# Kernel tuning notes

Measured on AMD Instinct MI355X. Metric: run time of the kernel, lower is better.

The kernel has to match this reference:

```python
import jax, jax.numpy as jnp
import numpy as np

DIM = 1024
HEADS = 16
HEAD_DIM = DIM // HEADS
RPE_K = 16
B, T = 4, 1024


def setup_inputs() -> dict:
    key = jax.random.key(0)
    ks = jax.random.split(key, 12)
    s = 1.0 / np.sqrt(DIM)
    inp = {
        'q': jax.random.normal(ks[0], (B, T, DIM), jnp.float32),
        'k': jax.random.normal(ks[1], (B, T, DIM), jnp.float32),
        'v': jax.random.normal(ks[2], (B, T, DIM), jnp.float32),
        'Wq': jax.random.normal(ks[3], (DIM, DIM), jnp.float32) * s,
        'bq': jnp.zeros((DIM,), jnp.float32),
        'Wk': jax.random.normal(ks[4], (DIM, DIM), jnp.float32) * s,
        'bk': jnp.zeros((DIM,), jnp.float32),
        'Wv': jax.random.normal(ks[5], (DIM, DIM), jnp.float32) * s,
        'bv': jnp.zeros((DIM,), jnp.float32),
        'rpe_w': jax.random.normal(ks[6], (2 * RPE_K + 1, 2 * HEAD_DIM), jnp.float32) * 0.02,
        'Wo': jax.random.normal(ks[7], (DIM, DIM), jnp.float32) * s,
        'bo': jnp.zeros((DIM,), jnp.float32),
    }
    return inp


def reference(q, k, v, Wq, bq, Wk, bk, Wv, bv, rpe_w, Wo, bo):
    b, ql = q.shape[:2]
    kl = k.shape[1]
    split = lambda x: x.reshape(b, -1, HEADS, HEAD_DIM).transpose(0, 2, 1, 3)  # b h t d
    qh = split(q @ Wq.T + bq)
    kh = split(k @ Wk.T + bk)
    vh = split(v @ Wv.T + bv)
    # note: original scales q BEFORE both the k-dot and the rpe_q einsum
    qh = qh / np.sqrt(HEAD_DIM)
    # relative distance table (constant ints)
    idx = jnp.arange(max(ql, kl))
    dist = jnp.clip(idx[:, None] - idx[None, :], -RPE_K, RPE_K) + RPE_K
    dist = dist[:ql, :kl]
    rpe = rpe_w[dist]                      # (ql, kl, 2*HEAD_DIM)
    rpe_q, rpe_v = jnp.split(rpe, 2, axis=-1)
    energy = jnp.einsum('bhqd,bhkd->bhqk', qh, kh)
    energy = energy + jnp.einsum('bhqd,qkd->bhqk', qh, rpe_q)
    alignment = jax.nn.softmax(energy, axis=-1)
    context = jnp.einsum('bhqk,bhkd->bhqd', alignment, vh)
    context = context + jnp.einsum('bhqk,qkd->bhqd', alignment, rpe_v)
    context = context.transpose(0, 2, 1, 3).reshape(b, ql, DIM)
    out = context @ Wo.T + bo
    return (out, alignment)
```

## Files before the change

kernel.cpp:

```cpp
#include <hip/hip_runtime.h>
#include <stdint.h>

typedef unsigned short u16;
typedef unsigned int   u32;
typedef short bf16x8 __attribute__((ext_vector_type(8)));
typedef float floatx4 __attribute__((ext_vector_type(4)));

#define OFF_XQ   0u
#define OFF_XK   4194304u
#define OFF_XV   8388608u
#define OFF_WQ   12582912u
#define OFF_WK   13631488u
#define OFF_WV   14680064u
#define OFF_WO   15728640u
#define OFF_QH   16777216u
#define OFF_KH   20971520u
#define OFF_VT   25165824u
#define OFF_CTX  29360128u

__device__ __forceinline__ u16 f2b(float f){
  u32 u = __float_as_uint(f);
  u = (u + 0x7fffu + ((u >> 16) & 1u)) >> 16;
  return (u16)u;
}
__device__ __forceinline__ float b2f(u16 h){
  return __uint_as_float(((u32)h) << 16);
}

__global__ __launch_bounds__(256) void convert_kernel(
    const float* __restrict__ q, const float* __restrict__ k, const float* __restrict__ v,
    const float* __restrict__ Wq, const float* __restrict__ Wk, const float* __restrict__ Wv,
    const float* __restrict__ Wo, u16* __restrict__ ws){
  int y = blockIdx.y;
  const float* src; u16* dst; int n;
  switch(y){
    case 0: src=q;  dst=ws+OFF_XQ; n=4194304; break;
    case 1: src=k;  dst=ws+OFF_XK; n=4194304; break;
    case 2: src=v;  dst=ws+OFF_XV; n=4194304; break;
    case 3: src=Wq; dst=ws+OFF_WQ; n=1048576; break;
    case 4: src=Wk; dst=ws+OFF_WK; n=1048576; break;
    case 5: src=Wv; dst=ws+OFF_WV; n=1048576; break;
    default:src=Wo; dst=ws+OFF_WO; n=1048576; break;
  }
  int idx = (blockIdx.x*256 + threadIdx.x)*4;
  if (idx >= n) return;
  float4 f = *(const float4*)(src + idx);
  ushort4 o;
  o.x = f2b(f.x); o.y = f2b(f.y); o.z = f2b(f.z); o.w = f2b(f.w);
  *(ushort4*)(dst + idx) = o;
}

template<int MODE>
__global__ __launch_bounds__(256) void gemm_kernel(
    const u16* __restrict__ A0, const u16* __restrict__ B0,
    const float* __restrict__ b0, const float* __restrict__ b1, const float* __restrict__ b2,
    u16* __restrict__ ws, float* __restrict__ outF){
  __shared__ u16 As[128][40];
  __shared__ u16 Bs[128][40];
  int z = (MODE==0) ? blockIdx.z : 0;
  const u16* A  = A0 + (size_t)z*4194304u;
  const u16* Bm = B0 + (size_t)z*1048576u;
  const float* bias = (MODE==0) ? (z==0?b0:(z==1?b1:b2)) : b0;
  int tid  = threadIdx.x;
  int lane = tid & 63, wave = tid >> 6;
  int wm = (wave>>1)*64, wn = (wave&1)*64;
  int m_base = blockIdx.y*128, n_base = blockIdx.x*128;
  floatx4 acc[4][4] = {};
  int fr = lane & 15, fo = (lane>>4)*8;
  for (int kb = 0; kb < 1024; kb += 32){
    #pragma unroll
    for (int p=0;p<2;p++){
      int L = tid + p*256;
      int row = L>>2, seg = (L&3)*8;
      *(uint4*)(&As[row][seg]) = *(const uint4*)(A  + (size_t)(m_base+row)*1024 + kb + seg);
      *(uint4*)(&Bs[row][seg]) = *(const uint4*)(Bm + (size_t)(n_base+row)*1024 + kb + seg);
    }
    __syncthreads();
    bf16x8 af[4], bfr[4];
    #pragma unroll
    for (int i=0;i<4;i++){
      af[i]  = *(const bf16x8*)(&As[wm + i*16 + fr][fo]);
      bfr[i] = *(const bf16x8*)(&Bs[wn + i*16 + fr][fo]);
    }
    #pragma unroll
    for (int i=0;i<4;i++)
      #pragma unroll
      for (int j=0;j<4;j++)
        acc[i][j] = __builtin_amdgcn_mfma_f32_16x16x32_bf16(af[i], bfr[j], acc[i][j], 0,0,0);
    __syncthreads();
  }
  int col = lane & 15, rb = (lane>>4)*4;
  #pragma unroll
  for (int i=0;i<4;i++){
    #pragma unroll
    for (int j=0;j<4;j++){
      int nn = n_base + wn + j*16 + col;
      float bv = bias[nn];
      #pragma unroll
      for (int r=0;r<4;r++){
        int mm = m_base + wm + i*16 + rb + r;
        float v = acc[i][j][r] + bv;
        if (MODE==0){
          if (z==0) v *= 0.125f;
          int b = mm>>10, t = mm&1023, h = nn>>6, d = nn&63;
          u32 base = (z==0)?OFF_QH:((z==1)?OFF_KH:OFF_VT);
          u32 idx = ((u32)(b*16+h))<<16;
          idx += (z==2) ? ((u32)(d<<10)+(u32)t) : ((u32)(t<<6)+(u32)d);
          ws[base + idx] = f2b(v);
        } else {
          outF[(size_t)mm*1024 + nn] = v;
        }
      }
    }
  }
}

__global__ __launch_bounds__(256) void attn_kernel(
    const u16* __restrict__ ws, const float* __restrict__ rpe_w,
    float* __restrict__ d_out, u16* __restrict__ ctx){
  __shared__ u16   P[16][1032];
  __shared__ u16   qs[16][64];
  __shared__ float proj[16][33];
  __shared__ float rpev[33][64];
  __shared__ float sacc[16][3];
  __shared__ float slds[16][33];
  __shared__ float linv[16];

  int bid = blockIdx.x;
  int qt = bid & 63, bh = bid >> 6;
  int q0 = qt * 16;
  int tid = threadIdx.x, lane = tid & 63, wave = tid >> 6;

  const u16* qh = ws + OFF_QH + (size_t)bh*65536;
  const u16* kh = ws + OFF_KH + (size_t)bh*65536;
  const u16* vT = ws + OFF_VT + (size_t)bh*65536;

  if (tid < 128){
    int r = tid >> 3, c = (tid & 7)*8;
    *(uint4*)(&qs[r][c]) = *(const uint4*)(qh + (size_t)(q0+r)*64 + c);
  }
  for (int i = tid; i < 33*64; i += 256){
    int t = i >> 6, d = i & 63;
    rpev[t][d] = rpe_w[t*128 + 64 + d];
  }
  if (tid < 48) ((float*)sacc)[tid] = 0.f;
  __syncthreads();

  for (int i = tid; i < 16*33; i += 256){
    int r = i / 33, t = i - r*33;
    float s = 0.f;
    #pragma unroll
    for (int d=0; d<64; d++) s += b2f(qs[r][d]) * rpe_w[t*128 + d];
    proj[r][t] = s;
  }
  __syncthreads();

  int col = lane & 15, rb = (lane>>4)*4, fo = (lane>>4)*8;
  bf16x8 aq0 = *(const bf16x8*)(&qs[col][fo]);
  bf16x8 aq1 = *(const bf16x8*)(&qs[col][32 + fo]);

  float tot[4] = {0,0,0,0}, lo[4] = {0,0,0,0}, hi[4] = {0,0,0,0};
  for (int kb = 0; kb < 1024; kb += 64){
    int key = kb + wave*16 + col;
    const u16* kp = kh + (size_t)key*64 + fo;
    bf16x8 bk0 = *(const bf16x8*)(kp);
    bf16x8 bk1 = *(const bf16x8*)(kp + 32);
    floatx4 s4 = {0.f,0.f,0.f,0.f};
    s4 = __builtin_amdgcn_mfma_f32_16x16x32_bf16(aq0, bk0, s4, 0,0,0);
    s4 = __builtin_amdgcn_mfma_f32_16x16x32_bf16(aq1, bk1, s4, 0,0,0);
    #pragma unroll
    for (int r=0;r<4;r++){
      int row = rb + r;
      int qg = q0 + row;
      int dd = qg - key;
      int bkt = min(max(dd, -16), 16) + 16;
      float p = __expf(s4[r] + proj[row][bkt]);
      P[row][key] = f2b(p);
      tot[r] += p;
      if      (key <= qg - 16) lo[r] += p;
      else if (key >= qg + 16) hi[r] += p;
    }
  }
  #pragma unroll
  for (int r=0;r<4;r++){
    #pragma unroll
    for (int m=8;m>=1;m>>=1){
      tot[r] += __shfl_xor(tot[r], m, 16);
      lo[r]  += __shfl_xor(lo[r],  m, 16);
      hi[r]  += __shfl_xor(hi[r],  m, 16);
    }
  }
  if (col == 0){
    #pragma unroll
    for (int r=0;r<4;r++){
      atomicAdd(&sacc[rb+r][0], tot[r]);
      atomicAdd(&sacc[rb+r][1], lo[r]);
      atomicAdd(&sacc[rb+r][2], hi[r]);
    }
  }
  __syncthreads();

  if (tid < 16){
    linv[tid] = 1.f / sacc[tid][0];
    slds[tid][32] = sacc[tid][1];
    slds[tid][0]  = sacc[tid][2];
  }
  for (int i = tid; i < 16*31; i += 256){
    int r = i / 31, t = 1 + (i - r*31);
    int kk = q0 + r + 16 - t;
    slds[r][t] = (kk >= 0 && kk < 1024) ? b2f(P[r][kk]) : 0.f;
  }
  __syncthreads();

  {
    int row = tid >> 4, c0 = (tid & 15)*4;
    float li = linv[row];
    float* outA = d_out + 4194304u + ((size_t)(bh*1024 + q0 + row))*1024;
    #pragma unroll
    for (int i=0;i<16;i++){
      int kcol = c0 + i*64;
      ushort4 pv = *(const ushort4*)(&P[row][kcol]);
      float4 o;
      o.x = b2f(pv.x)*li; o.y = b2f(pv.y)*li;
      o.z = b2f(pv.z)*li; o.w = b2f(pv.w)*li;
      *(float4*)(outA + kcol) = o;
    }
  }

  floatx4 o4 = {0.f,0.f,0.f,0.f};
  int n0 = wave*16;
  {
    const u16* vbase = vT + (size_t)(n0 + col)*1024;
    for (int kk = 0; kk < 1024; kk += 32){
      bf16x8 ap  = *(const bf16x8*)(&P[col][kk + fo]);
      bf16x8 bv8 = *(const bf16x8*)(vbase + kk + fo);
      o4 = __builtin_amdgcn_mfma_f32_16x16x32_bf16(ap, bv8, o4, 0,0,0);
    }
  }
  {
    int b = bh >> 4, h = bh & 15;
    #pragma unroll
    for (int r=0;r<4;r++){
      int row = rb + r;
      int d = n0 + col;
      float sv = 0.f;
      #pragma unroll
      for (int t=0;t<33;t++) sv += slds[row][t]*rpev[t][d];
      float v = (o4[r] + sv) * linv[row];
      ctx[((size_t)(b*1024 + q0 + row))*1024 + h*64 + d] = f2b(v);
    }
  }
}

extern "C" void kernel_launch(void* const* d_in, const int* in_sizes, int n_in,
                              void* d_out, int out_size, void* d_ws, size_t ws_size,
                              hipStream_t stream){
  const float* q  = (const float*)d_in[0];
  const float* k  = (const float*)d_in[1];
  const float* v  = (const float*)d_in[2];
  const float* Wq = (const float*)d_in[3];
  const float* bq = (const float*)d_in[4];
  const float* Wk = (const float*)d_in[5];
  const float* bk = (const float*)d_in[6];
  const float* Wv = (const float*)d_in[7];
  const float* bv = (const float*)d_in[8];
  const float* rpe= (const float*)d_in[9];
  const float* Wo = (const float*)d_in[10];
  const float* bo = (const float*)d_in[11];
  u16* ws = (u16*)d_ws;
  float* out = (float*)d_out;

  convert_kernel<<<dim3(4096,7), 256, 0, stream>>>(q,k,v,Wq,Wk,Wv,Wo, ws);
  gemm_kernel<0><<<dim3(8,32,3), 256, 0, stream>>>(ws+OFF_XQ, ws+OFF_WQ, bq, bk, bv, ws, nullptr);
  attn_kernel<<<dim3(4096), 256, 0, stream>>>(ws, rpe, out, ws+OFF_CTX);
  gemm_kernel<1><<<dim3(8,32), 256, 0, stream>>>(ws+OFF_CTX, ws+OFF_WO, bo, nullptr, nullptr, ws, out);
}
```

Baseline: 604.0 us.

## Recompute attention scores in second pass and use direct global-to-LDS GEMM loads

The attention kernel no longer keeps the full 16x1024 probability row in LDS. It computes row sums in a first pass, then recomputes the scores in a second pass and streams the normalized probabilities straight to global memory. That second pass feeds P·V through a small double-buffered, XOR-swizzled LDS tile, which cuts LDS footprint to allow more occupancy. The cost is repeating the QK MFMA and exp work and adding a block barrier per 64-key chunk. The GEMM tile loads now use global_load_lds with unpadded shared arrays, which drops the register round-trip but may add LDS bank conflicts on the fragment reads.

```diff
diff --git a/kernel.cpp b/kernel.cpp
--- a/kernel.cpp
+++ b/kernel.cpp
@@ -55,8 +55,8 @@
     const u16* __restrict__ A0, const u16* __restrict__ B0,
     const float* __restrict__ b0, const float* __restrict__ b1, const float* __restrict__ b2,
     u16* __restrict__ ws, float* __restrict__ outF){
-  __shared__ u16 As[128][40];
-  __shared__ u16 Bs[128][40];
+  __shared__ u16 As[128][32];
+  __shared__ u16 Bs[128][32];
   int z = (MODE==0) ? blockIdx.z : 0;
   const u16* A  = A0 + (size_t)z*4194304u;
   const u16* Bm = B0 + (size_t)z*1048576u;
@@ -67,14 +67,20 @@
   int m_base = blockIdx.y*128, n_base = blockIdx.x*128;
   floatx4 acc[4][4] = {};
   int fr = lane & 15, fo = (lane>>4)*8;
+  int srow = lane >> 2, sseg = (lane & 3)*8;
+  u16* AsW0 = &As[wave*32][0];
+  u16* AsW1 = &As[wave*32+16][0];
+  u16* BsW0 = &Bs[wave*32][0];
+  u16* BsW1 = &Bs[wave*32+16][0];
+  const u16* Ag0 = A  + (size_t)(m_base + wave*32      + srow)*1024 + sseg;
+  const u16* Ag1 = A  + (size_t)(m_base + wave*32 + 16 + srow)*1024 + sseg;
+  const u16* Bg0 = Bm + (size_t)(n_base + wave*32      + srow)*1024 + sseg;
+  const u16* Bg1 = Bm + (size_t)(n_base + wave*32 + 16 + srow)*1024 + sseg;
   for (int kb = 0; kb < 1024; kb += 32){
-    #pragma unroll
-    for (int p=0;p<2;p++){
-      int L = tid + p*256;
-      int row = L>>2, seg = (L&3)*8;
-      *(uint4*)(&As[row][seg]) = *(const uint4*)(A  + (size_t)(m_base+row)*1024 + kb + seg);
-      *(uint4*)(&Bs[row][seg]) = *(const uint4*)(Bm + (size_t)(n_base+row)*1024 + kb + seg);
-    }
+    __builtin_amdgcn_global_load_lds((const u32*)(Ag0 + kb), (u32*)AsW0, 16, 0, 0);
+    __builtin_amdgcn_global_load_lds((const u32*)(Ag1 + kb), (u32*)AsW1, 16, 0, 0);
+    __builtin_amdgcn_global_load_lds((const u32*)(Bg0 + kb), (u32*)BsW0, 16, 0, 0);
+    __builtin_amdgcn_global_load_lds((const u32*)(Bg1 + kb), (u32*)BsW1, 16, 0, 0);
     __syncthreads();
     bf16x8 af[4], bfr[4];
     #pragma unroll
@@ -118,13 +124,13 @@
 __global__ __launch_bounds__(256) void attn_kernel(
     const u16* __restrict__ ws, const float* __restrict__ rpe_w,
     float* __restrict__ d_out, u16* __restrict__ ctx){
-  __shared__ u16   P[16][1032];
   __shared__ u16   qs[16][64];
   __shared__ float proj[16][33];
+  __shared__ u16   Pt[2][1024];
   __shared__ float rpev[33][64];
   __shared__ float sacc[16][3];
   __shared__ float slds[16][33];
-  __shared__ float linv[16];
+  __shared__ float linv16[16];
 
   int bid = blockIdx.x;
   int qt = bid & 63, bh = bid >> 6;
@@ -144,6 +150,7 @@
     rpev[t][d] = rpe_w[t*128 + 64 + d];
   }
   if (tid < 48) ((float*)sacc)[tid] = 0.f;
+  for (int i = tid; i < 16*33; i += 256) ((float*)slds)[i] = 0.f;
   __syncthreads();
 
   for (int i = tid; i < 16*33; i += 256){
@@ -160,8 +167,9 @@
   bf16x8 aq1 = *(const bf16x8*)(&qs[col][32 + fo]);
 
   float tot[4] = {0,0,0,0}, lo[4] = {0,0,0,0}, hi[4] = {0,0,0,0};
+  int kl = wave*16 + col;
   for (int kb = 0; kb < 1024; kb += 64){
-    int key = kb + wave*16 + col;
+    int key = kb + kl;
     const u16* kp = kh + (size_t)key*64 + fo;
     bf16x8 bk0 = *(const bf16x8*)(kp);
     bf16x8 bk1 = *(const bf16x8*)(kp + 32);
@@ -170,12 +178,9 @@
     s4 = __builtin_amdgcn_mfma_f32_16x16x32_bf16(aq1, bk1, s4, 0,0,0);
     #pragma unroll
     for (int r=0;r<4;r++){
-      int row = rb + r;
-      int qg = q0 + row;
-      int dd = qg - key;
+      int row = rb + r, qg = q0 + row, dd = qg - key;
       int bkt = min(max(dd, -16), 16) + 16;
       float p = __expf(s4[r] + proj[row][bkt]);
-      P[row][key] = f2b(p);
       tot[r] += p;
       if      (key <= qg - 16) lo[r] += p;
       else if (key >= qg + 16) hi[r] += p;
@@ -201,52 +206,60 @@
   __syncthreads();
 
   if (tid < 16){
-    linv[tid] = 1.f / sacc[tid][0];
+    linv16[tid] = 1.f / sacc[tid][0];
     slds[tid][32] = sacc[tid][1];
     slds[tid][0]  = sacc[tid][2];
   }
-  for (int i = tid; i < 16*31; i += 256){
-    int r = i / 31, t = 1 + (i - r*31);
-    int kk = q0 + r + 16 - t;
-    slds[r][t] = (kk >= 0 && kk < 1024) ? b2f(P[r][kk]) : 0.f;
-  }
-  __syncthreads();
-
-  {
-    int row = tid >> 4, c0 = (tid & 15)*4;
-    float li = linv[row];
-    float* outA = d_out + 4194304u + ((size_t)(bh*1024 + q0 + row))*1024;
-    #pragma unroll
-    for (int i=0;i<16;i++){
-      int kcol = c0 + i*64;
-      ushort4 pv = *(const ushort4*)(&P[row][kcol]);
-      float4 o;
-      o.x = b2f(pv.x)*li; o.y = b2f(pv.y)*li;
-      o.z = b2f(pv.z)*li; o.w = b2f(pv.w)*li;
-      *(float4*)(outA + kcol) = o;
-    }
-  }
+  __syncthreads();
+
+  float li[4];
+  #pragma unroll
+  for (int r=0;r<4;r++) li[r] = linv16[rb+r];
 
   floatx4 o4 = {0.f,0.f,0.f,0.f};
-  int n0 = wave*16;
-  {
-    const u16* vbase = vT + (size_t)(n0 + col)*1024;
-    for (int kk = 0; kk < 1024; kk += 32){
-      bf16x8 ap  = *(const bf16x8*)(&P[col][kk + fo]);
-      bf16x8 bv8 = *(const bf16x8*)(vbase + kk + fo);
-      o4 = __builtin_amdgcn_mfma_f32_16x16x32_bf16(ap, bv8, o4, 0,0,0);
-    }
-  }
+  int n0w = wave*16;
+  const u16* vbase = vT + (size_t)(n0w + col)*1024;
+  float* outA = d_out + 4194304u + ((size_t)(bh*1024 + q0))*1024;
+  int swr = (col&7)<<3;
+  for (int it = 0; it < 16; ++it){
+    int kb = it*64;
+    int key = kb + kl;
+    int buf = it & 1;
+    const u16* kp = kh + (size_t)key*64 + fo;
+    bf16x8 bk0 = *(const bf16x8*)(kp);
+    bf16x8 bk1 = *(const bf16x8*)(kp + 32);
+    floatx4 s4 = {0.f,0.f,0.f,0.f};
+    s4 = __builtin_amdgcn_mfma_f32_16x16x32_bf16(aq0, bk0, s4, 0,0,0);
+    s4 = __builtin_amdgcn_mfma_f32_16x16x32_bf16(aq1, bk1, s4, 0,0,0);
+    #pragma unroll
+    for (int r=0;r<4;r++){
+      int row = rb + r, qg = q0 + row, dd = qg - key;
+      int bkt = min(max(dd, -16), 16) + 16;
+      float p = __expf(s4[r] + proj[row][bkt]);
+      Pt[buf][row*64 + (kl ^ ((row&7)<<3))] = f2b(p);
+      if (dd > -16 && dd < 16) slds[row][dd+16] = p;
+      outA[(size_t)row*1024 + key] = p * li[r];
+    }
+    __syncthreads();
+    bf16x8 ap0 = *(const bf16x8*)(&Pt[buf][col*64 + (fo ^ swr)]);
+    bf16x8 ap1 = *(const bf16x8*)(&Pt[buf][col*64 + ((fo+32) ^ swr)]);
+    bf16x8 bv0 = *(const bf16x8*)(vbase + kb + fo);
+    bf16x8 bv1 = *(const bf16x8*)(vbase + kb + 32 + fo);
+    o4 = __builtin_amdgcn_mfma_f32_16x16x32_bf16(ap0, bv0, o4, 0,0,0);
+    o4 = __builtin_amdgcn_mfma_f32_16x16x32_bf16(ap1, bv1, o4, 0,0,0);
+  }
+  __syncthreads();
+
   {
     int b = bh >> 4, h = bh & 15;
     #pragma unroll
     for (int r=0;r<4;r++){
       int row = rb + r;
-      int d = n0 + col;
+      int d = n0w + col;
       float sv = 0.f;
       #pragma unroll
       for (int t=0;t<33;t++) sv += slds[row][t]*rpev[t][d];
-      float v = (o4[r] + sv) * linv[row];
+      float v = (o4[r] + sv) * li[r];
       ctx[((size_t)(b*1024 + q0 + row))*1024 + h*64 + d] = f2b(v);
     }
   }
```

New measurement: 654.9 us. +8.4%, slower.
